# Kernel optimization log

Hardware: AMD Instinct MI355X
Metric: run time of the kernel (lower is better)

## Reference

```python
import jax, jax.numpy as jnp
import numpy as np

DIM = 128
HEADS = 4
NS = 7          # neighborhood_size (odd)
RADIUS = NS // 2
EXP = 2         # ffn expansion
EPS = 1e-8


def rmsnorm(x, w):
    # x: [B,C,H,W], w: [1,C,1,1]
    rms = jnp.mean(jnp.square(x), axis=1, keepdims=True)
    return x * jax.lax.rsqrt(rms + EPS) * w


def conv1x1(x, w, b):
    # w: [Cout,Cin], b: [Cout]
    return jnp.einsum('oi,bihw->bohw', w, x) + b[None, :, None, None]


def setup_inputs() -> dict:
    key = jax.random.key(0)
    ks = jax.random.split(key, 20)
    B, C, H, W = 2, DIM, 64, 64
    s = 0.02
    d = {
        'z': jax.random.normal(ks[0], (B, C, H, W), jnp.float32),
        'h': jax.random.normal(ks[1], (B, C, H, W), jnp.float32),
        'wz_norm': jnp.ones((1, C, 1, 1), jnp.float32),
        'wh_norm': jnp.ones((1, C, 1, 1), jnp.float32),
        'wq': jax.random.normal(ks[2], (C, C), jnp.float32) * s,
        'bq': jnp.zeros((C,), jnp.float32),
        'wk': jax.random.normal(ks[3], (C, C), jnp.float32) * s,
        'bk': jnp.zeros((C,), jnp.float32),
        'wv': jax.random.normal(ks[4], (C, C), jnp.float32) * s,
        'bv': jnp.zeros((C,), jnp.float32),
        'wo': jax.random.normal(ks[5], (C, C), jnp.float32) * s,
        'bo': jnp.zeros((C,), jnp.float32),
        'wffn_norm': jnp.ones((1, C, 1, 1), jnp.float32),
        'w1': jax.random.normal(ks[6], (C * EXP, C), jnp.float32) * s,
        'b1': jnp.zeros((C * EXP,), jnp.float32),
        'w2': jax.random.normal(ks[7], (C, C * EXP), jnp.float32) * s,
        'b2': jnp.zeros((C,), jnp.float32),
    }
    return d


def neighborhood_cross_attn(zq, hk, wq, bq, wk, bk, wv, bv, wo, bo):
    B, C, H, W = zq.shape
    hd = C // HEADS
    scale = hd ** (-0.5)
    q = conv1x1(zq, wq, bq)
    k = conv1x1(hk, wk, bk)
    v = conv1x1(hk, wv, bv)
    # [B, heads, H, W, hd]
    qh = q.reshape(B, HEADS, hd, H, W).transpose(0, 1, 3, 4, 2)
    kh = k.reshape(B, HEADS, hd, H, W).transpose(0, 1, 3, 4, 2)
    vh = v.reshape(B, HEADS, hd, H, W).transpose(0, 1, 3, 4, 2)
    offs = jnp.arange(-RADIUS, RADIUS + 1)
    dy, dx = jnp.meshgrid(offs, offs, indexing='ij')
    dy = dy.reshape(-1)  # [K]
    dx = dx.reshape(-1)
    by, bx = jnp.meshgrid(jnp.arange(H), jnp.arange(W), indexing='ij')
    ny = by[:, :, None] + dy  # [H, W, K]
    nx = bx[:, :, None] + dx
    valid = (ny >= 0) & (ny < H) & (nx >= 0) & (nx < W)
    nyc = jnp.clip(ny, 0, H - 1)
    nxc = jnp.clip(nx, 0, W - 1)
    # gather neighbors: [B, heads, H, W, K, hd]
    k_nb = kh[:, :, nyc, nxc]
    v_nb = vh[:, :, nyc, nxc]
    attn = jnp.einsum('bnhwd,bnhwkd->bnhwk', qh, k_nb) * scale
    attn = jnp.where(valid[None, None], attn, jnp.finfo(attn.dtype).min)
    p = jax.nn.softmax(attn, axis=-1)
    out = jnp.einsum('bnhwk,bnhwkd->bnhwd', p, v_nb)
    out = out.transpose(0, 1, 4, 2, 3).reshape(B, C, H, W)
    return conv1x1(out, wo, bo)


def reference(z, h, wz_norm, wh_norm, wq, bq, wk, bk, wv, bv, wo, bo,
              wffn_norm, w1, b1, w2, b2):
    h_norm = rmsnorm(h, wh_norm)
    z_norm = rmsnorm(z, wz_norm)
    z = z + neighborhood_cross_attn(z_norm, h_norm, wq, bq, wk, bk, wv, bv, wo, bo)
    y = rmsnorm(z, wffn_norm)
    y = conv1x1(y, w1, b1)
    y = jax.nn.gelu(y, approximate=False)
    y = conv1x1(y, w2, b2)
    return z + y
```

## Files before the change

### kernel.cpp

```cpp
#include <hip/hip_runtime.h>
#include <math.h>

#define CDIM 128
#define HW   4096
#define HEADS 4
#define HD   32

typedef __attribute__((ext_vector_type(8))) short bf16x8;
typedef __attribute__((ext_vector_type(4))) float f32x4;

static __device__ __forceinline__ unsigned int f2bf(float f) {
  union { float f; unsigned int u; } v; v.f = f;
  unsigned int r = v.u + 0x7FFF + ((v.u >> 16) & 1);
  return r >> 16;
}
static __device__ __forceinline__ float bflo(unsigned int u) {
  return __uint_as_float(u << 16);
}
static __device__ __forceinline__ float bfhi(unsigned int u) {
  return __uint_as_float(u & 0xFFFF0000u);
}
static __device__ __forceinline__ float gelu_f(float v) {
  return 0.5f * v * (1.0f + erff(v * 0.70710678118654752f));
}

__global__ __launch_bounds__(256) void head(
    const float* __restrict__ z, const float* __restrict__ h,
    const float* __restrict__ wzn, const float* __restrict__ whn,
    const float* __restrict__ wq, const float* __restrict__ bq,
    const float* __restrict__ wk, const float* __restrict__ bk,
    const float* __restrict__ wv, const float* __restrict__ bv,
    const float* __restrict__ wo, const float* __restrict__ w1,
    const float* __restrict__ w2, ushort* __restrict__ WB,
    ushort* __restrict__ Qb, ushort* __restrict__ Kb, ushort* __restrict__ Vb) {
  const int sel = blockIdx.y, t = threadIdx.x;
  if (sel == 3) {
    int e = (blockIdx.x * 256 + t) * 4;
    if (e < 81920) {
      const float* src; int off;
      if      (e < 16384) { src = wo; off = 0; }
      else if (e < 49152) { src = w1; off = 16384; }
      else                { src = w2; off = 49152; }
      float4 v = *(const float4*)&src[e - off];
      uint2 r;
      r.x = f2bf(v.x) | (f2bf(v.y) << 16);
      r.y = f2bf(v.z) | (f2bf(v.w) << 16);
      *(uint2*)&WB[49152 + e] = r;
    }
    return;
  }
  __shared__ __align__(16) ushort sW[128 * 128];
  __shared__ __align__(16) ushort sX[64 * 128];
  __shared__ float sh[4][64];

  const float* X    = (sel == 0) ? z : h;
  const float* wn   = (sel == 0) ? wzn : whn;
  const float* Wf   = (sel == 0) ? wq : (sel == 1 ? wk : wv);
  const float* bias = (sel == 0) ? bq : (sel == 1 ? bk : bv);
  ushort* outB      = (sel == 0) ? Qb : (sel == 1 ? Kb : Vb);

#pragma unroll
  for (int i = 0; i < 8; ++i) {
    int u  = t + i * 256;
    int o  = u >> 4;
    int k8 = (u & 15) * 8;
    float4 v0 = *(const float4*)&Wf[o * 128 + k8];
    float4 v1 = *(const float4*)&Wf[o * 128 + k8 + 4];
    uint4 pk;
    pk.x = f2bf(v0.x) | (f2bf(v0.y) << 16);
    pk.y = f2bf(v0.z) | (f2bf(v0.w) << 16);
    pk.z = f2bf(v1.x) | (f2bf(v1.y) << 16);
    pk.w = f2bf(v1.z) | (f2bf(v1.w) << 16);
    int idx = (o * 128 + k8) ^ ((o & 7) << 3);
    *(uint4*)&sW[idx] = pk;
  }

  const int pl = t & 63, g = t >> 6;
  const int gp = blockIdx.x * 64 + pl;
  const size_t xbase = (size_t)(gp >> 12) * CDIM * HW + (gp & 4095);
  float vals[32];
  float ss = 0.f;
#pragma unroll
  for (int j = 0; j < 32; ++j) {
    float v = X[xbase + (size_t)(g * 32 + j) * HW];
    vals[j] = v;
    ss += v * v;
  }
  sh[g][pl] = ss;
  __syncthreads();
  float tot = sh[0][pl] + sh[1][pl] + sh[2][pl] + sh[3][pl];
  float inv = rsqrtf(tot * (1.0f / CDIM) + 1e-8f);
#pragma unroll
  for (int jj = 0; jj < 4; ++jj) {
    unsigned int u[4];
#pragma unroll
    for (int p2 = 0; p2 < 4; ++p2) {
      int j = jj * 8 + p2 * 2;
      float a = vals[j]     * inv * wn[g * 32 + j];
      float b = vals[j + 1] * inv * wn[g * 32 + j + 1];
      u[p2] = f2bf(a) | (f2bf(b) << 16);
    }
    int idx = (pl * 128 + g * 32 + jj * 8) ^ ((pl & 7) << 3);
    *(uint4*)&sX[idx] = make_uint4(u[0], u[1], u[2], u[3]);
  }
  __syncthreads();

  const int w = t >> 6, l = t & 63, lr = l & 15, lk = l >> 4;
  const int m0 = w * 32;
  const int swz = (lr & 7) << 3;
  f32x4 acc[2][4] = {};
#pragma unroll
  for (int k0 = 0; k0 < 128; k0 += 32) {
    bf16x8 a0 = *(const bf16x8*)&sW[((m0 + lr) * 128 + k0 + lk * 8) ^ swz];
    bf16x8 a1 = *(const bf16x8*)&sW[((m0 + 16 + lr) * 128 + k0 + lk * 8) ^ swz];
    bf16x8 b[4];
#pragma unroll
    for (int nf = 0; nf < 4; ++nf)
      b[nf] = *(const bf16x8*)&sX[((nf * 16 + lr) * 128 + k0 + lk * 8) ^ swz];
#pragma unroll
    for (int nf = 0; nf < 4; ++nf) {
      acc[0][nf] = __builtin_amdgcn_mfma_f32_16x16x32_bf16(a0, b[nf], acc[0][nf], 0, 0, 0);
      acc[1][nf] = __builtin_amdgcn_mfma_f32_16x16x32_bf16(a1, b[nf], acc[1][nf], 0, 0, 0);
    }
  }
#pragma unroll
  for (int mf = 0; mf < 2; ++mf) {
    int obase = m0 + mf * 16 + lk * 4;
    f32x4 bv = *(const f32x4*)&bias[obase];
#pragma unroll
    for (int nf = 0; nf < 4; ++nf) {
      int P = blockIdx.x * 64 + nf * 16 + lr;
      uint2 pk;
      pk.x = f2bf(acc[mf][nf][0] + bv[0]) | (f2bf(acc[mf][nf][1] + bv[1]) << 16);
      pk.y = f2bf(acc[mf][nf][2] + bv[2]) | (f2bf(acc[mf][nf][3] + bv[3]) << 16);
      *(uint2*)&outB[(size_t)P * CDIM + obase] = pk;
    }
  }
}

__global__ __launch_bounds__(512) void nattn(
    const ushort* __restrict__ Q, const ushort* __restrict__ K,
    const ushort* __restrict__ V, ushort* __restrict__ ATT) {
  __shared__ __align__(16) unsigned int smem[20480];
  float* sS = (float*)smem;
  const int t  = threadIdx.x;
  const int px = t & 127;
  const int x  = px & 63;
  const int r  = px >> 6;
  const int dg = t >> 7;
  const int y0 = blockIdx.x * 2;
  const int h  = blockIdx.y;
  const int b  = blockIdx.z;
  const int ybase = y0 - 3;

  {
    int yy = t >> 6, xs = t & 63;
    int gy = min(max(ybase + yy, 0), 63);
    size_t gb = ((size_t)(b * HW + gy * 64 + xs)) * 64 + h * 16;
    const unsigned int* Ku = (const unsigned int*)K;
    const unsigned int* Vu = (const unsigned int*)V;
    int lb = (yy * 64 + xs) * 20;
#pragma unroll
    for (int i = 0; i < 4; ++i) {
      uint4 kv = *(const uint4*)&Ku[gb + i * 4];
      uint4 vv = *(const uint4*)&Vu[gb + i * 4];
      *(uint4*)&smem[lb + i * 4]         = kv;
      *(uint4*)&smem[10240 + lb + i * 4] = vv;
    }
  }
  const int Pq = b * HW + (y0 + r) * 64 + x;
  const unsigned int* Qu = (const unsigned int*)Q;
  float q[32];
#pragma unroll
  for (int i = 0; i < 4; ++i) {
    uint4 u4 = *(const uint4*)&Qu[(size_t)Pq * 64 + h * 16 + i * 4];
    q[i*8+0] = bflo(u4.x); q[i*8+1] = bfhi(u4.x);
    q[i*8+2] = bflo(u4.y); q[i*8+3] = bfhi(u4.y);
    q[i*8+4] = bflo(u4.z); q[i*8+5] = bfhi(u4.z);
    q[i*8+6] = bflo(u4.w); q[i*8+7] = bfhi(u4.w);
  }
  __syncthreads();

  const float scale = 0.17677669529663687f;
  const int nb0    = (dg == 0) ? 0 : dg * 12 + 1;
  const int ncount = (dg == 0) ? 13 : 12;
  float sreg[13];
#pragma unroll
  for (int j = 0; j < 13; ++j) {
    if (j < ncount) {
      int nb = nb0 + j;
      int dy = nb / 7 - 3;
      int dx = nb % 7 - 3;
      int ry = r + dy + 3;
      int nx = x + dx;
      int xx = min(max(nx, 0), 63);
      int ny = y0 + r + dy;
      bool valid = (ny >= 0) && (ny <= 63) && (nx >= 0) && (nx <= 63);
      const unsigned int* kb = &smem[(ry * 64 + xx) * 20];
      float acc = 0.f;
#pragma unroll
      for (int c = 0; c < 4; ++c) {
        uint4 u4 = *(const uint4*)&kb[c * 4];
        acc += q[c*8+0] * bflo(u4.x) + q[c*8+1] * bfhi(u4.x);
        acc += q[c*8+2] * bflo(u4.y) + q[c*8+3] * bfhi(u4.y);
        acc += q[c*8+4] * bflo(u4.z) + q[c*8+5] * bfhi(u4.z);
        acc += q[c*8+6] * bflo(u4.w) + q[c*8+7] * bfhi(u4.w);
      }
      sreg[j] = valid ? acc * scale : -1e30f;
    }
  }
  __syncthreads();
#pragma unroll
  for (int j = 0; j < 13; ++j)
    if (j < ncount) sS[(nb0 + j) * 128 + px] = sreg[j];
  __syncthreads();

  float o[8] = {0.f, 0.f, 0.f, 0.f, 0.f, 0.f, 0.f, 0.f};
  float sum = 0.f;
#pragma unroll
  for (int nb = 0; nb < 49; ++nb) {
    float p = __expf(sS[nb * 128 + px] - 8.0f);
    sum += p;
    int ry = r + nb / 7;
    int xx = min(max(x + nb % 7 - 3, 0), 63);
    uint4 u4 = *(const uint4*)&smem[10240 + (ry * 64 + xx) * 20 + dg * 4];
    o[0] += p * bflo(u4.x); o[1] += p * bfhi(u4.x);
    o[2] += p * bflo(u4.y); o[3] += p * bfhi(u4.y);
    o[4] += p * bflo(u4.z); o[5] += p * bfhi(u4.z);
    o[6] += p * bflo(u4.w); o[7] += p * bfhi(u4.w);
  }
  float inv = 1.0f / sum;
  unsigned int pk[4];
#pragma unroll
  for (int j = 0; j < 4; ++j)
    pk[j] = f2bf(o[2*j] * inv) | (f2bf(o[2*j+1] * inv) << 16);
  *(uint4*)&ATT[(size_t)Pq * CDIM + h * HD + dg * 8] = make_uint4(pk[0], pk[1], pk[2], pk[3]);
}

__global__ __launch_bounds__(256) void tail(
    const ushort* __restrict__ ATT, const ushort* __restrict__ WB,
    const float* __restrict__ bo, const float* __restrict__ z,
    const float* __restrict__ wfn, const float* __restrict__ b1,
    const float* __restrict__ b2, float* __restrict__ out) {
  __shared__ __align__(16) float  zlds[32][132];
  __shared__ __align__(16) ushort fn_s[32 * 128];
  __shared__ __align__(16) ushort hid_s[32 * 256];
  __shared__ float sums[32][17];
  __shared__ float sinv[32];
  const ushort* Wo = WB + 49152;
  const ushort* W1 = WB + 65536;
  const ushort* W2 = WB + 98304;
  const int t = threadIdx.x, w = t >> 6, l = t & 63, lr = l & 15, lk = l >> 4;
  const int pblk = blockIdx.x * 32;
  const int m0 = w * 32;

  {
    const ushort* A0 = Wo + (size_t)(m0 + lr) * 128 + lk * 8;
    const ushort* A1 = A0 + 16 * 128;
    const ushort* B0 = ATT + (size_t)(pblk + lr) * 128 + lk * 8;
    const ushort* B1 = B0 + 16 * 128;
    f32x4 acc[2][2] = {};
#pragma unroll
    for (int k0 = 0; k0 < 128; k0 += 32) {
      bf16x8 a0 = *(const bf16x8*)(A0 + k0);
      bf16x8 a1 = *(const bf16x8*)(A1 + k0);
      bf16x8 b0 = *(const bf16x8*)(B0 + k0);
      bf16x8 b1 = *(const bf16x8*)(B1 + k0);
      acc[0][0] = __builtin_amdgcn_mfma_f32_16x16x32_bf16(a0, b0, acc[0][0], 0, 0, 0);
      acc[0][1] = __builtin_amdgcn_mfma_f32_16x16x32_bf16(a0, b1, acc[0][1], 0, 0, 0);
      acc[1][0] = __builtin_amdgcn_mfma_f32_16x16x32_bf16(a1, b0, acc[1][0], 0, 0, 0);
      acc[1][1] = __builtin_amdgcn_mfma_f32_16x16x32_bf16(a1, b1, acc[1][1], 0, 0, 0);
    }
#pragma unroll
    for (int nf = 0; nf < 2; ++nf) {
      int px = nf * 16 + lr;
      int P  = pblk + px;
      int b_ = P >> 12, p = P & 4095;
      float ss = 0.f;
#pragma unroll
      for (int mf = 0; mf < 2; ++mf) {
        int row0 = m0 + mf * 16 + lk * 4;
        f32x4 bv = *(const f32x4*)&bo[row0];
        f32x4 rr;
#pragma unroll
        for (int j = 0; j < 4; ++j) {
          size_t gi = ((size_t)(b_ * CDIM + row0 + j)) * HW + p;
          float u = acc[mf][nf][j] + bv[j] + z[gi];
          rr[j] = u;
          ss += u * u;
        }
        *(f32x4*)&zlds[px][row0] = rr;
      }
      sums[px][w * 4 + lk] = ss;
    }
  }
  __syncthreads();
  if (t < 32) {
    float tot = 0.f;
#pragma unroll
    for (int i = 0; i < 16; ++i) tot += sums[t][i];
    sinv[t] = rsqrtf(tot * (1.0f / CDIM) + 1e-8f);
  }
  __syncthreads();
#pragma unroll
  for (int nf = 0; nf < 2; ++nf) {
    int px = nf * 16 + lr;
    float inv = sinv[px];
#pragma unroll
    for (int mf = 0; mf < 2; ++mf) {
      int row0 = m0 + mf * 16 + lk * 4;
      f32x4 uu = *(const f32x4*)&zlds[px][row0];
      f32x4 wf = *(const f32x4*)&wfn[row0];
      uint2 pk;
      pk.x = f2bf(uu[0] * inv * wf[0]) | (f2bf(uu[1] * inv * wf[1]) << 16);
      pk.y = f2bf(uu[2] * inv * wf[2]) | (f2bf(uu[3] * inv * wf[3]) << 16);
      int idx = (px * 128 + row0) ^ ((px & 7) << 3);
      *(uint2*)&fn_s[idx] = pk;
    }
  }
  __syncthreads();
  {
    const int hm0 = w * 64;
    const ushort* A0 = W1 + (size_t)(hm0 + lr) * 128 + lk * 8;
    f32x4 acc1[4][2] = {};
#pragma unroll
    for (int k0 = 0; k0 < 128; k0 += 32) {
      bf16x8 a[4], b[2];
#pragma unroll
      for (int mf = 0; mf < 4; ++mf) a[mf] = *(const bf16x8*)(A0 + mf * 16 * 128 + k0);
#pragma unroll
      for (int nf = 0; nf < 2; ++nf) {
        int px = nf * 16 + lr;
        b[nf] = *(const bf16x8*)&fn_s[(px * 128 + k0 + lk * 8) ^ ((px & 7) << 3)];
      }
#pragma unroll
      for (int mf = 0; mf < 4; ++mf)
#pragma unroll
        for (int nf = 0; nf < 2; ++nf)
          acc1[mf][nf] = __builtin_amdgcn_mfma_f32_16x16x32_bf16(a[mf], b[nf], acc1[mf][nf], 0, 0, 0);
    }
#pragma unroll
    for (int mf = 0; mf < 4; ++mf) {
      int ch0 = hm0 + mf * 16 + lk * 4;
      f32x4 bv = *(const f32x4*)&b1[ch0];
#pragma unroll
      for (int nf = 0; nf < 2; ++nf) {
        int px = nf * 16 + lr;
        float v0 = gelu_f(acc1[mf][nf][0] + bv[0]);
        float v1 = gelu_f(acc1[mf][nf][1] + bv[1]);
        float v2 = gelu_f(acc1[mf][nf][2] + bv[2]);
        float v3 = gelu_f(acc1[mf][nf][3] + bv[3]);
        uint2 pk;
        pk.x = f2bf(v0) | (f2bf(v1) << 16);
        pk.y = f2bf(v2) | (f2bf(v3) << 16);
        int idx = (px * 256 + ch0) ^ ((px & 7) << 3);
        *(uint2*)&hid_s[idx] = pk;
      }
    }
  }
  __syncthreads();
  {
    const ushort* C0 = W2 + (size_t)(m0 + lr) * 256 + lk * 8;
    f32x4 acc2[2][2] = {};
#pragma unroll
    for (int k0 = 0; k0 < 256; k0 += 32) {
      bf16x8 a0 = *(const bf16x8*)(C0 + k0);
      bf16x8 a1 = *(const bf16x8*)(C0 + 16 * 256 + k0);
      bf16x8 b[2];
#pragma unroll
      for (int nf = 0; nf < 2; ++nf) {
        int px = nf * 16 + lr;
        b[nf] = *(const bf16x8*)&hid_s[(px * 256 + k0 + lk * 8) ^ ((px & 7) << 3)];
      }
      acc2[0][0] = __builtin_amdgcn_mfma_f32_16x16x32_bf16(a0, b[0], acc2[0][0], 0, 0, 0);
      acc2[0][1] = __builtin_amdgcn_mfma_f32_16x16x32_bf16(a0, b[1], acc2[0][1], 0, 0, 0);
      acc2[1][0] = __builtin_amdgcn_mfma_f32_16x16x32_bf16(a1, b[0], acc2[1][0], 0, 0, 0);
      acc2[1][1] = __builtin_amdgcn_mfma_f32_16x16x32_bf16(a1, b[1], acc2[1][1], 0, 0, 0);
    }
#pragma unroll
    for (int mf = 0; mf < 2; ++mf) {
      int row0 = m0 + mf * 16 + lk * 4;
      f32x4 bv = *(const f32x4*)&b2[row0];
#pragma unroll
      for (int nf = 0; nf < 2; ++nf) {
        int px = nf * 16 + lr;
        int P  = pblk + px;
        int b_ = P >> 12, p = P & 4095;
        f32x4 zz = *(const f32x4*)&zlds[px][row0];
#pragma unroll
        for (int j = 0; j < 4; ++j) {
          size_t gi = ((size_t)(b_ * CDIM + row0 + j)) * HW + p;
          out[gi] = acc2[mf][nf][j] + bv[j] + zz[j];
        }
      }
    }
  }
}

extern "C" void kernel_launch(void* const* d_in, const int* in_sizes, int n_in,
                              void* d_out, int out_size, void* d_ws, size_t ws_size,
                              hipStream_t stream) {
  const float* z   = (const float*)d_in[0];
  const float* h   = (const float*)d_in[1];
  const float* wzn = (const float*)d_in[2];
  const float* whn = (const float*)d_in[3];
  const float* wq  = (const float*)d_in[4];
  const float* bq  = (const float*)d_in[5];
  const float* wk  = (const float*)d_in[6];
  const float* bk  = (const float*)d_in[7];
  const float* wv  = (const float*)d_in[8];
  const float* bv  = (const float*)d_in[9];
  const float* wo  = (const float*)d_in[10];
  const float* bo  = (const float*)d_in[11];
  const float* wfn = (const float*)d_in[12];
  const float* w1  = (const float*)d_in[13];
  const float* b1  = (const float*)d_in[14];
  const float* w2  = (const float*)d_in[15];
  const float* b2  = (const float*)d_in[16];
  float* out = (float*)d_out;

  const size_t U = 1048576;
  ushort* Qb  = (ushort*)d_ws;
  ushort* Kb  = Qb + U;
  ushort* Vb  = Kb + U;
  ushort* ATT = Vb + U;
  ushort* WB  = ATT + U;

  head<<<dim3(128, 4), 256, 0, stream>>>(z, h, wzn, whn, wq, bq, wk, bk, wv, bv,
                                         wo, w1, w2, WB, Qb, Kb, Vb);
  nattn<<<dim3(32, HEADS, 2), 512, 0, stream>>>(Qb, Kb, Vb, ATT);
  tail<<<dim3(256), 256, 0, stream>>>(ATT, WB, bo, z, wfn, b1, b2, out);
}
```

Measured before the change: 40.59 us.

## Fuse three kernels into one persistent kernel with grid barriers

Merges the projection, neighborhood-attention and FFN tail kernels into a single 256-block, 512-thread kernel. Stages are separated by software grid-wide atomic barriers, and a memset resets the counters before each launch. This removes two kernel launch gaps, and the tail stage is re-tiled so each wave computes 16 output rows instead of 32. It also moves the softmax exp into the score loop and replaces erf GELU with a sigmoid-based tanh approximation, which changes numerics slightly. The barrier relies on all 256 blocks being co-resident, and it adds a memset launch.

Result: slower. 90.58 us (+123.2%).

```diff
diff --git a/kernel.cpp b/kernel.cpp
--- a/kernel.cpp
+++ b/kernel.cpp
@@ -3,7 +3,6 @@
 
 #define CDIM 128
 #define HW   4096
-#define HEADS 4
 #define HD   32
 
 typedef __attribute__((ext_vector_type(8))) short bf16x8;
@@ -21,365 +20,362 @@
   return __uint_as_float(u & 0xFFFF0000u);
 }
 static __device__ __forceinline__ float gelu_f(float v) {
-  return 0.5f * v * (1.0f + erff(v * 0.70710678118654752f));
-}
-
-__global__ __launch_bounds__(256) void head(
+  float y = v * (1.595769122f + 0.071354816f * v * v);
+  return v / (1.0f + __expf(-y));
+}
+
+static __device__ __forceinline__ void gridbar(unsigned int* c, unsigned int n) {
+  __syncthreads();
+  if (threadIdx.x == 0) {
+    __threadfence();
+    atomicAdd(c, 1u);
+    while (__hip_atomic_load(c, __ATOMIC_RELAXED, __HIP_MEMORY_SCOPE_AGENT) < n) {}
+    __threadfence();
+  }
+  __syncthreads();
+}
+
+__global__ __launch_bounds__(512) void fused(
     const float* __restrict__ z, const float* __restrict__ h,
     const float* __restrict__ wzn, const float* __restrict__ whn,
     const float* __restrict__ wq, const float* __restrict__ bq,
     const float* __restrict__ wk, const float* __restrict__ bk,
     const float* __restrict__ wv, const float* __restrict__ bv,
-    const float* __restrict__ wo, const float* __restrict__ w1,
-    const float* __restrict__ w2, ushort* __restrict__ WB,
-    ushort* __restrict__ Qb, ushort* __restrict__ Kb, ushort* __restrict__ Vb) {
-  const int sel = blockIdx.y, t = threadIdx.x;
-  if (sel == 3) {
-    int e = (blockIdx.x * 256 + t) * 4;
-    if (e < 81920) {
+    const float* __restrict__ wo, const float* __restrict__ bo,
+    const float* __restrict__ wfn, const float* __restrict__ w1,
+    const float* __restrict__ b1, const float* __restrict__ w2,
+    const float* __restrict__ b2,
+    ushort* __restrict__ Qb, ushort* __restrict__ Kb, ushort* __restrict__ Vb,
+    ushort* __restrict__ ATT, ushort* __restrict__ WB,
+    float* __restrict__ out, unsigned int* __restrict__ bar) {
+  __shared__ __align__(16) unsigned char SMEM[100352];
+  const int t   = threadIdx.x;
+  const int bid = blockIdx.x;
+
+  {
+    const int g   = t >> 8;
+    const int t2  = t & 255;
+    const int job = bid * 2 + g;
+    const int type = job >> 7;
+    ushort* sW = (ushort*)(SMEM + g * 32768);
+    ushort* sX = (ushort*)(SMEM + 65536 + g * 16384);
+    float*  sh = (float*)(SMEM + 98304 + g * 1024);
+    const int pxb = job & 127;
+    const int pl = t2 & 63, gq = t2 >> 6;
+    float vals[32];
+
+    if (type < 3) {
+      const float* Wf = (type == 0) ? wq : (type == 1 ? wk : wv);
+#pragma unroll
+      for (int i = 0; i < 8; ++i) {
+        int u  = t2 + i * 256;
+        int o  = u >> 4;
+        int k8 = (u & 15) * 8;
+        float4 v0 = *(const float4*)&Wf[o * 128 + k8];
+        float4 v1 = *(const float4*)&Wf[o * 128 + k8 + 4];
+        uint4 pk;
+        pk.x = f2bf(v0.x) | (f2bf(v0.y) << 16);
+        pk.y = f2bf(v0.z) | (f2bf(v0.w) << 16);
+        pk.z = f2bf(v1.x) | (f2bf(v1.y) << 16);
+        pk.w = f2bf(v1.z) | (f2bf(v1.w) << 16);
+        *(uint4*)&sW[(o * 128 + k8) ^ ((o & 7) << 3)] = pk;
+      }
+      const float* X = (type == 0) ? z : h;
+      const int gp = pxb * 64 + pl;
+      const size_t xbase = (size_t)(gp >> 12) * CDIM * HW + (gp & 4095);
+      float ss = 0.f;
+#pragma unroll
+      for (int j = 0; j < 32; ++j) {
+        float v = X[xbase + (size_t)(gq * 32 + j) * HW];
+        vals[j] = v;
+        ss += v * v;
+      }
+      sh[gq * 64 + pl] = ss;
+    } else if (job - 384 < 80) {
+      int e = ((job - 384) * 256 + t2) * 4;
       const float* src; int off;
       if      (e < 16384) { src = wo; off = 0; }
       else if (e < 49152) { src = w1; off = 16384; }
       else                { src = w2; off = 49152; }
       float4 v = *(const float4*)&src[e - off];
-      uint2 r;
-      r.x = f2bf(v.x) | (f2bf(v.y) << 16);
-      r.y = f2bf(v.z) | (f2bf(v.w) << 16);
-      *(uint2*)&WB[49152 + e] = r;
-    }
-    return;
+      uint2 r2;
+      r2.x = f2bf(v.x) | (f2bf(v.y) << 16);
+      r2.y = f2bf(v.z) | (f2bf(v.w) << 16);
+      *(uint2*)&WB[49152 + e] = r2;
+    }
+    __syncthreads();
+    if (type < 3) {
+      const float* wn = (type == 0) ? wzn : whn;
+      float tot = sh[pl] + sh[64 + pl] + sh[128 + pl] + sh[192 + pl];
+      float inv = rsqrtf(tot * (1.0f / CDIM) + 1e-8f);
+#pragma unroll
+      for (int jj = 0; jj < 4; ++jj) {
+        unsigned int u[4];
+#pragma unroll
+        for (int p2 = 0; p2 < 4; ++p2) {
+          int j = jj * 8 + p2 * 2;
+          float a = vals[j]     * inv * wn[gq * 32 + j];
+          float b = vals[j + 1] * inv * wn[gq * 32 + j + 1];
+          u[p2] = f2bf(a) | (f2bf(b) << 16);
+        }
+        int idx = (pl * 128 + gq * 32 + jj * 8) ^ ((pl & 7) << 3);
+        *(uint4*)&sX[idx] = make_uint4(u[0], u[1], u[2], u[3]);
+      }
+    }
+    __syncthreads();
+    if (type < 3) {
+      const int w4 = t2 >> 6, l = t2 & 63, lr = l & 15, lk = l >> 4;
+      const int m0 = w4 * 32;
+      const int swz = (lr & 7) << 3;
+      const float* bias = (type == 0) ? bq : (type == 1 ? bk : bv);
+      ushort* outB      = (type == 0) ? Qb : (type == 1 ? Kb : Vb);
+      f32x4 acc[2][4] = {};
+#pragma unroll
+      for (int ki = 0; ki < 4; ++ki) {
+        bf16x8 a0 = *(const bf16x8*)&sW[((m0 + lr) * 128 + ki * 32 + lk * 8) ^ swz];
+        bf16x8 a1 = *(const bf16x8*)&sW[((m0 + 16 + lr) * 128 + ki * 32 + lk * 8) ^ swz];
+#pragma unroll
+        for (int nf = 0; nf < 4; ++nf) {
+          bf16x8 bb = *(const bf16x8*)&sX[((nf * 16 + lr) * 128 + ki * 32 + lk * 8) ^ swz];
+          acc[0][nf] = __builtin_amdgcn_mfma_f32_16x16x32_bf16(a0, bb, acc[0][nf], 0, 0, 0);
+          acc[1][nf] = __builtin_amdgcn_mfma_f32_16x16x32_bf16(a1, bb, acc[1][nf], 0, 0, 0);
+        }
+      }
+#pragma unroll
+      for (int mf = 0; mf < 2; ++mf) {
+        int obase = m0 + mf * 16 + lk * 4;
+        f32x4 bv4 = *(const f32x4*)&bias[obase];
+#pragma unroll
+        for (int nf = 0; nf < 4; ++nf) {
+          int P = pxb * 64 + nf * 16 + lr;
+          uint2 pk;
+          pk.x = f2bf(acc[mf][nf][0] + bv4[0]) | (f2bf(acc[mf][nf][1] + bv4[1]) << 16);
+          pk.y = f2bf(acc[mf][nf][2] + bv4[2]) | (f2bf(acc[mf][nf][3] + bv4[3]) << 16);
+          *(uint2*)&outB[(size_t)P * CDIM + obase] = pk;
+        }
+      }
+    }
   }
-  __shared__ __align__(16) ushort sW[128 * 128];
-  __shared__ __align__(16) ushort sX[64 * 128];
-  __shared__ float sh[4][64];
-
-  const float* X    = (sel == 0) ? z : h;
-  const float* wn   = (sel == 0) ? wzn : whn;
-  const float* Wf   = (sel == 0) ? wq : (sel == 1 ? wk : wv);
-  const float* bias = (sel == 0) ? bq : (sel == 1 ? bk : bv);
-  ushort* outB      = (sel == 0) ? Qb : (sel == 1 ? Kb : Vb);
-
-#pragma unroll
-  for (int i = 0; i < 8; ++i) {
-    int u  = t + i * 256;
-    int o  = u >> 4;
-    int k8 = (u & 15) * 8;
-    float4 v0 = *(const float4*)&Wf[o * 128 + k8];
-    float4 v1 = *(const float4*)&Wf[o * 128 + k8 + 4];
-    uint4 pk;
-    pk.x = f2bf(v0.x) | (f2bf(v0.y) << 16);
-    pk.y = f2bf(v0.z) | (f2bf(v0.w) << 16);
-    pk.z = f2bf(v1.x) | (f2bf(v1.y) << 16);
-    pk.w = f2bf(v1.z) | (f2bf(v1.w) << 16);
-    int idx = (o * 128 + k8) ^ ((o & 7) << 3);
-    *(uint4*)&sW[idx] = pk;
+  gridbar(&bar[0], gridDim.x);
+
+  {
+    unsigned int* smem = (unsigned int*)SMEM;
+    float* sS = (float*)smem;
+    const int px = t & 127;
+    const int x  = px & 63;
+    const int r  = px >> 6;
+    const int dg = t >> 7;
+    const int y0 = (bid & 31) * 2;
+    const int hh = (bid >> 5) & 3;
+    const int b  = bid >> 7;
+    const int ybase = y0 - 3;
+    {
+      int yy = t >> 6, xs = t & 63;
+      int gy = min(max(ybase + yy, 0), 63);
+      size_t gb = ((size_t)(b * HW + gy * 64 + xs)) * 64 + hh * 16;
+      const unsigned int* Ku = (const unsigned int*)Kb;
+      const unsigned int* Vu = (const unsigned int*)Vb;
+      int lb = (yy * 64 + xs) * 20;
+#pragma unroll
+      for (int i = 0; i < 4; ++i) {
+        uint4 kv = *(const uint4*)&Ku[gb + i * 4];
+        uint4 vv = *(const uint4*)&Vu[gb + i * 4];
+        *(uint4*)&smem[lb + i * 4]         = kv;
+        *(uint4*)&smem[10240 + lb + i * 4] = vv;
+      }
+    }
+    const int Pq = b * HW + (y0 + r) * 64 + x;
+    const unsigned int* Qu = (const unsigned int*)Qb;
+    float q[32];
+#pragma unroll
+    for (int i = 0; i < 4; ++i) {
+      uint4 u4 = *(const uint4*)&Qu[(size_t)Pq * 64 + hh * 16 + i * 4];
+      q[i*8+0] = bflo(u4.x); q[i*8+1] = bfhi(u4.x);
+      q[i*8+2] = bflo(u4.y); q[i*8+3] = bfhi(u4.y);
+      q[i*8+4] = bflo(u4.z); q[i*8+5] = bfhi(u4.z);
+      q[i*8+6] = bflo(u4.w); q[i*8+7] = bfhi(u4.w);
+    }
+    __syncthreads();
+    const float scale = 0.17677669529663687f;
+    const int nb0    = (dg == 0) ? 0 : dg * 12 + 1;
+    const int ncount = (dg == 0) ? 13 : 12;
+    float sreg[13];
+#pragma unroll
+    for (int j = 0; j < 13; ++j) {
+      if (j < ncount) {
+        int nb = nb0 + j;
+        int dy = nb / 7 - 3;
+        int dx = nb % 7 - 3;
+        int ry = r + dy + 3;
+        int nx = x + dx;
+        int xx = min(max(nx, 0), 63);
+        int ny = y0 + r + dy;
+        bool valid = (ny >= 0) && (ny <= 63) && (nx >= 0) && (nx <= 63);
+        const unsigned int* kb = &smem[(ry * 64 + xx) * 20];
+        float acc = 0.f;
+#pragma unroll
+        for (int c = 0; c < 4; ++c) {
+          uint4 u4 = *(const uint4*)&kb[c * 4];
+          acc += q[c*8+0] * bflo(u4.x) + q[c*8+1] * bfhi(u4.x);
+          acc += q[c*8+2] * bflo(u4.y) + q[c*8+3] * bfhi(u4.y);
+          acc += q[c*8+4] * bflo(u4.z) + q[c*8+5] * bfhi(u4.z);
+          acc += q[c*8+6] * bflo(u4.w) + q[c*8+7] * bfhi(u4.w);
+        }
+        sreg[j] = valid ? __expf(acc * scale - 8.0f) : 0.0f;
+      }
+    }
+    __syncthreads();
+#pragma unroll
+    for (int j = 0; j < 13; ++j)
+      if (j < ncount) sS[(nb0 + j) * 128 + px] = sreg[j];
+    __syncthreads();
+    float o[8] = {0.f, 0.f, 0.f, 0.f, 0.f, 0.f, 0.f, 0.f};
+    float sum = 0.f;
+#pragma unroll
+    for (int nb = 0; nb < 49; ++nb) {
+      float p = sS[nb * 128 + px];
+      sum += p;
+      int ry = r + nb / 7;
+      int xx = min(max(x + nb % 7 - 3, 0), 63);
+      uint4 u4 = *(const uint4*)&smem[10240 + (ry * 64 + xx) * 20 + dg * 4];
+      o[0] += p * bflo(u4.x); o[1] += p * bfhi(u4.x);
+      o[2] += p * bflo(u4.y); o[3] += p * bfhi(u4.y);
+      o[4] += p * bflo(u4.z); o[5] += p * bfhi(u4.z);
+      o[6] += p * bflo(u4.w); o[7] += p * bfhi(u4.w);
+    }
+    float inv = 1.0f / sum;
+    unsigned int pk[4];
+#pragma unroll
+    for (int j = 0; j < 4; ++j)
+      pk[j] = f2bf(o[2*j] * inv) | (f2bf(o[2*j+1] * inv) << 16);
+    *(uint4*)&ATT[(size_t)Pq * CDIM + hh * HD + dg * 8] = make_uint4(pk[0], pk[1], pk[2], pk[3]);
   }
-
-  const int pl = t & 63, g = t >> 6;
-  const int gp = blockIdx.x * 64 + pl;
-  const size_t xbase = (size_t)(gp >> 12) * CDIM * HW + (gp & 4095);
-  float vals[32];
-  float ss = 0.f;
-#pragma unroll
-  for (int j = 0; j < 32; ++j) {
-    float v = X[xbase + (size_t)(g * 32 + j) * HW];
-    vals[j] = v;
-    ss += v * v;
-  }
-  sh[g][pl] = ss;
-  __syncthreads();
-  float tot = sh[0][pl] + sh[1][pl] + sh[2][pl] + sh[3][pl];
-  float inv = rsqrtf(tot * (1.0f / CDIM) + 1e-8f);
-#pragma unroll
-  for (int jj = 0; jj < 4; ++jj) {
-    unsigned int u[4];
-#pragma unroll
-    for (int p2 = 0; p2 < 4; ++p2) {
-      int j = jj * 8 + p2 * 2;
-      float a = vals[j]     * inv * wn[g * 32 + j];
-      float b = vals[j + 1] * inv * wn[g * 32 + j + 1];
-      u[p2] = f2bf(a) | (f2bf(b) << 16);
-    }
-    int idx = (pl * 128 + g * 32 + jj * 8) ^ ((pl & 7) << 3);
-    *(uint4*)&sX[idx] = make_uint4(u[0], u[1], u[2], u[3]);
-  }
-  __syncthreads();
-
-  const int w = t >> 6, l = t & 63, lr = l & 15, lk = l >> 4;
-  const int m0 = w * 32;
-  const int swz = (lr & 7) << 3;
-  f32x4 acc[2][4] = {};
-#pragma unroll
-  for (int k0 = 0; k0 < 128; k0 += 32) {
-    bf16x8 a0 = *(const bf16x8*)&sW[((m0 + lr) * 128 + k0 + lk * 8) ^ swz];
-    bf16x8 a1 = *(const bf16x8*)&sW[((m0 + 16 + lr) * 128 + k0 + lk * 8) ^ swz];
-    bf16x8 b[4];
-#pragma unroll
-    for (int nf = 0; nf < 4; ++nf)
-      b[nf] = *(const bf16x8*)&sX[((nf * 16 + lr) * 128 + k0 + lk * 8) ^ swz];
-#pragma unroll
-    for (int nf = 0; nf < 4; ++nf) {
-      acc[0][nf] = __builtin_amdgcn_mfma_f32_16x16x32_bf16(a0, b[nf], acc[0][nf], 0, 0, 0);
-      acc[1][nf] = __builtin_amdgcn_mfma_f32_16x16x32_bf16(a1, b[nf], acc[1][nf], 0, 0, 0);
-    }
-  }
-#pragma unroll
-  for (int mf = 0; mf < 2; ++mf) {
-    int obase = m0 + mf * 16 + lk * 4;
-    f32x4 bv = *(const f32x4*)&bias[obase];
-#pragma unroll
-    for (int nf = 0; nf < 4; ++nf) {
-      int P = blockIdx.x * 64 + nf * 16 + lr;
-      uint2 pk;
-      pk.x = f2bf(acc[mf][nf][0] + bv[0]) | (f2bf(acc[mf][nf][1] + bv[1]) << 16);
-      pk.y = f2bf(acc[mf][nf][2] + bv[2]) | (f2bf(acc[mf][nf][3] + bv[3]) << 16);
-      *(uint2*)&outB[(size_t)P * CDIM + obase] = pk;
-    }
-  }
-}
-
-__global__ __launch_bounds__(512) void nattn(
-    const ushort* __restrict__ Q, const ushort* __restrict__ K,
-    const ushort* __restrict__ V, ushort* __restrict__ ATT) {
-  __shared__ __align__(16) unsigned int smem[20480];
-  float* sS = (float*)smem;
-  const int t  = threadIdx.x;
-  const int px = t & 127;
-  const int x  = px & 63;
-  const int r  = px >> 6;
-  const int dg = t >> 7;
-  const int y0 = blockIdx.x * 2;
-  const int h  = blockIdx.y;
-  const int b  = blockIdx.z;
-  const int ybase = y0 - 3;
+  gridbar(&bar[1], gridDim.x);
 
   {
-    int yy = t >> 6, xs = t & 63;
-    int gy = min(max(ybase + yy, 0), 63);
-    size_t gb = ((size_t)(b * HW + gy * 64 + xs)) * 64 + h * 16;
-    const unsigned int* Ku = (const unsigned int*)K;
-    const unsigned int* Vu = (const unsigned int*)V;
-    int lb = (yy * 64 + xs) * 20;
-#pragma unroll
-    for (int i = 0; i < 4; ++i) {
-      uint4 kv = *(const uint4*)&Ku[gb + i * 4];
-      uint4 vv = *(const uint4*)&Vu[gb + i * 4];
-      *(uint4*)&smem[lb + i * 4]         = kv;
-      *(uint4*)&smem[10240 + lb + i * 4] = vv;
-    }
-  }
-  const int Pq = b * HW + (y0 + r) * 64 + x;
-  const unsigned int* Qu = (const unsigned int*)Q;
-  float q[32];
-#pragma unroll
-  for (int i = 0; i < 4; ++i) {
-    uint4 u4 = *(const uint4*)&Qu[(size_t)Pq * 64 + h * 16 + i * 4];
-    q[i*8+0] = bflo(u4.x); q[i*8+1] = bfhi(u4.x);
-    q[i*8+2] = bflo(u4.y); q[i*8+3] = bfhi(u4.y);
-    q[i*8+4] = bflo(u4.z); q[i*8+5] = bfhi(u4.z);
-    q[i*8+6] = bflo(u4.w); q[i*8+7] = bfhi(u4.w);
-  }
-  __syncthreads();
-
-  const float scale = 0.17677669529663687f;
-  const int nb0    = (dg == 0) ? 0 : dg * 12 + 1;
-  const int ncount = (dg == 0) ? 13 : 12;
-  float sreg[13];
-#pragma unroll
-  for (int j = 0; j < 13; ++j) {
-    if (j < ncount) {
-      int nb = nb0 + j;
-      int dy = nb / 7 - 3;
-      int dx = nb % 7 - 3;
-      int ry = r + dy + 3;
-      int nx = x + dx;
-      int xx = min(max(nx, 0), 63);
-      int ny = y0 + r + dy;
-      bool valid = (ny >= 0) && (ny <= 63) && (nx >= 0) && (nx <= 63);
-      const unsigned int* kb = &smem[(ry * 64 + xx) * 20];
-      float acc = 0.f;
-#pragma unroll
-      for (int c = 0; c < 4; ++c) {
-        uint4 u4 = *(const uint4*)&kb[c * 4];
-        acc += q[c*8+0] * bflo(u4.x) + q[c*8+1] * bfhi(u4.x);
-        acc += q[c*8+2] * bflo(u4.y) + q[c*8+3] * bfhi(u4.y);
-        acc += q[c*8+4] * bflo(u4.z) + q[c*8+5] * bfhi(u4.z);
-        acc += q[c*8+6] * bflo(u4.w) + q[c*8+7] * bfhi(u4.w);
-      }
-      sreg[j] = valid ? acc * scale : -1e30f;
-    }
-  }
-  __syncthreads();
-#pragma unroll
-  for (int j = 0; j < 13; ++j)
-    if (j < ncount) sS[(nb0 + j) * 128 + px] = sreg[j];
-  __syncthreads();
-
-  float o[8] = {0.f, 0.f, 0.f, 0.f, 0.f, 0.f, 0.f, 0.f};
-  float sum = 0.f;
-#pragma unroll
-  for (int nb = 0; nb < 49; ++nb) {
-    float p = __expf(sS[nb * 128 + px] - 8.0f);
-    sum += p;
-    int ry = r + nb / 7;
-    int xx = min(max(x + nb % 7 - 3, 0), 63);
-    uint4 u4 = *(const uint4*)&smem[10240 + (ry * 64 + xx) * 20 + dg * 4];
-    o[0] += p * bflo(u4.x); o[1] += p * bfhi(u4.x);
-    o[2] += p * bflo(u4.y); o[3] += p * bfhi(u4.y);
-    o[4] += p * bflo(u4.z); o[5] += p * bfhi(u4.z);
-    o[6] += p * bflo(u4.w); o[7] += p * bfhi(u4.w);
-  }
-  float inv = 1.0f / sum;
-  unsigned int pk[4];
-#pragma unroll
-  for (int j = 0; j < 4; ++j)
-    pk[j] = f2bf(o[2*j] * inv) | (f2bf(o[2*j+1] * inv) << 16);
-  *(uint4*)&ATT[(size_t)Pq * CDIM + h * HD + dg * 8] = make_uint4(pk[0], pk[1], pk[2], pk[3]);
-}
-
-__global__ __launch_bounds__(256) void tail(
-    const ushort* __restrict__ ATT, const ushort* __restrict__ WB,
-    const float* __restrict__ bo, const float* __restrict__ z,
-    const float* __restrict__ wfn, const float* __restrict__ b1,
-    const float* __restrict__ b2, float* __restrict__ out) {
-  __shared__ __align__(16) float  zlds[32][132];
-  __shared__ __align__(16) ushort fn_s[32 * 128];
-  __shared__ __align__(16) ushort hid_s[32 * 256];
-  __shared__ float sums[32][17];
-  __shared__ float sinv[32];
-  const ushort* Wo = WB + 49152;
-  const ushort* W1 = WB + 65536;
-  const ushort* W2 = WB + 98304;
-  const int t = threadIdx.x, w = t >> 6, l = t & 63, lr = l & 15, lk = l >> 4;
-  const int pblk = blockIdx.x * 32;
-  const int m0 = w * 32;
-
-  {
-    const ushort* A0 = Wo + (size_t)(m0 + lr) * 128 + lk * 8;
-    const ushort* A1 = A0 + 16 * 128;
-    const ushort* B0 = ATT + (size_t)(pblk + lr) * 128 + lk * 8;
-    const ushort* B1 = B0 + 16 * 128;
-    f32x4 acc[2][2] = {};
-#pragma unroll
-    for (int k0 = 0; k0 < 128; k0 += 32) {
-      bf16x8 a0 = *(const bf16x8*)(A0 + k0);
-      bf16x8 a1 = *(const bf16x8*)(A1 + k0);
-      bf16x8 b0 = *(const bf16x8*)(B0 + k0);
-      bf16x8 b1 = *(const bf16x8*)(B1 + k0);
-      acc[0][0] = __builtin_amdgcn_mfma_f32_16x16x32_bf16(a0, b0, acc[0][0], 0, 0, 0);
-      acc[0][1] = __builtin_amdgcn_mfma_f32_16x16x32_bf16(a0, b1, acc[0][1], 0, 0, 0);
-      acc[1][0] = __builtin_amdgcn_mfma_f32_16x16x32_bf16(a1, b0, acc[1][0], 0, 0, 0);
-      acc[1][1] = __builtin_amdgcn_mfma_f32_16x16x32_bf16(a1, b1, acc[1][1], 0, 0, 0);
-    }
-#pragma unroll
-    for (int nf = 0; nf < 2; ++nf) {
-      int px = nf * 16 + lr;
-      int P  = pblk + px;
-      int b_ = P >> 12, p = P & 4095;
-      float ss = 0.f;
-#pragma unroll
-      for (int mf = 0; mf < 2; ++mf) {
-        int row0 = m0 + mf * 16 + lk * 4;
-        f32x4 bv = *(const f32x4*)&bo[row0];
+    float  (*zlds)[132] = (float(*)[132])SMEM;
+    ushort* fn_s  = (ushort*)(SMEM + 16896);
+    ushort* hid_s = (ushort*)(SMEM + 25088);
+    float  (*sums)[36] = (float(*)[36])(SMEM + 41472);
+    float*  sinv  = (float*)(SMEM + 46080);
+    const ushort* Wo = WB + 49152;
+    const ushort* W1 = WB + 65536;
+    const ushort* W2 = WB + 98304;
+    const int w = t >> 6, l = t & 63, lr = l & 15, lk = l >> 4;
+    const int pblk = bid * 32;
+    {
+      const int m0 = w * 16;
+      const ushort* A0 = Wo + (size_t)(m0 + lr) * 128 + lk * 8;
+      const ushort* B0 = ATT + (size_t)(pblk + lr) * 128 + lk * 8;
+      const ushort* B1 = B0 + 16 * 128;
+      f32x4 acc[2] = {};
+#pragma unroll
+      for (int k0 = 0; k0 < 128; k0 += 32) {
+        bf16x8 a0 = *(const bf16x8*)(A0 + k0);
+        bf16x8 b0 = *(const bf16x8*)(B0 + k0);
+        bf16x8 b1 = *(const bf16x8*)(B1 + k0);
+        acc[0] = __builtin_amdgcn_mfma_f32_16x16x32_bf16(a0, b0, acc[0], 0, 0, 0);
+        acc[1] = __builtin_amdgcn_mfma_f32_16x16x32_bf16(a0, b1, acc[1], 0, 0, 0);
+      }
+      const int row0 = m0 + lk * 4;
+      f32x4 bv = *(const f32x4*)&bo[row0];
+#pragma unroll
+      for (int nf = 0; nf < 2; ++nf) {
+        int px = nf * 16 + lr;
+        int P  = pblk + px;
+        int b_ = P >> 12, p = P & 4095;
+        float ss = 0.f;
         f32x4 rr;
 #pragma unroll
         for (int j = 0; j < 4; ++j) {
           size_t gi = ((size_t)(b_ * CDIM + row0 + j)) * HW + p;
-          float u = acc[mf][nf][j] + bv[j] + z[gi];
+          float u = acc[nf][j] + bv[j] + z[gi];
           rr[j] = u;
           ss += u * u;
         }
         *(f32x4*)&zlds[px][row0] = rr;
-      }
-      sums[px][w * 4 + lk] = ss;
-    }
-  }
-  __syncthreads();
-  if (t < 32) {
-    float tot = 0.f;
-#pragma unroll
-    for (int i = 0; i < 16; ++i) tot += sums[t][i];
-    sinv[t] = rsqrtf(tot * (1.0f / CDIM) + 1e-8f);
-  }
-  __syncthreads();
-#pragma unroll
-  for (int nf = 0; nf < 2; ++nf) {
-    int px = nf * 16 + lr;
-    float inv = sinv[px];
-#pragma unroll
-    for (int mf = 0; mf < 2; ++mf) {
-      int row0 = m0 + mf * 16 + lk * 4;
-      f32x4 uu = *(const f32x4*)&zlds[px][row0];
+        sums[px][w * 4 + lk] = ss;
+      }
+    }
+    __syncthreads();
+    if (t < 32) {
+      float tot = 0.f;
+#pragma unroll
+      for (int i = 0; i < 32; ++i) tot += sums[t][i];
+      sinv[t] = rsqrtf(tot * (1.0f / CDIM) + 1e-8f);
+    }
+    __syncthreads();
+    {
+      const int row0 = w * 16 + lk * 4;
       f32x4 wf = *(const f32x4*)&wfn[row0];
-      uint2 pk;
-      pk.x = f2bf(uu[0] * inv * wf[0]) | (f2bf(uu[1] * inv * wf[1]) << 16);
-      pk.y = f2bf(uu[2] * inv * wf[2]) | (f2bf(uu[3] * inv * wf[3]) << 16);
-      int idx = (px * 128 + row0) ^ ((px & 7) << 3);
-      *(uint2*)&fn_s[idx] = pk;
-    }
-  }
-  __syncthreads();
-  {
-    const int hm0 = w * 64;
-    const ushort* A0 = W1 + (size_t)(hm0 + lr) * 128 + lk * 8;
-    f32x4 acc1[4][2] = {};
-#pragma unroll
-    for (int k0 = 0; k0 < 128; k0 += 32) {
-      bf16x8 a[4], b[2];
-#pragma unroll
-      for (int mf = 0; mf < 4; ++mf) a[mf] = *(const bf16x8*)(A0 + mf * 16 * 128 + k0);
 #pragma unroll
       for (int nf = 0; nf < 2; ++nf) {
         int px = nf * 16 + lr;
-        b[nf] = *(const bf16x8*)&fn_s[(px * 128 + k0 + lk * 8) ^ ((px & 7) << 3)];
-      }
-#pragma unroll
-      for (int mf = 0; mf < 4; ++mf)
-#pragma unroll
-        for (int nf = 0; nf < 2; ++nf)
-          acc1[mf][nf] = __builtin_amdgcn_mfma_f32_16x16x32_bf16(a[mf], b[nf], acc1[mf][nf], 0, 0, 0);
-    }
-#pragma unroll
-    for (int mf = 0; mf < 4; ++mf) {
-      int ch0 = hm0 + mf * 16 + lk * 4;
-      f32x4 bv = *(const f32x4*)&b1[ch0];
-#pragma unroll
-      for (int nf = 0; nf < 2; ++nf) {
-        int px = nf * 16 + lr;
-        float v0 = gelu_f(acc1[mf][nf][0] + bv[0]);
-        float v1 = gelu_f(acc1[mf][nf][1] + bv[1]);
-        float v2 = gelu_f(acc1[mf][nf][2] + bv[2]);
-        float v3 = gelu_f(acc1[mf][nf][3] + bv[3]);
+        float inv = sinv[px];
+        f32x4 uu = *(const f32x4*)&zlds[px][row0];
         uint2 pk;
-        pk.x = f2bf(v0) | (f2bf(v1) << 16);
-        pk.y = f2bf(v2) | (f2bf(v3) << 16);
-        int idx = (px * 256 + ch0) ^ ((px & 7) << 3);
-        *(uint2*)&hid_s[idx] = pk;
-      }
-    }
-  }
-  __syncthreads();
-  {
-    const ushort* C0 = W2 + (size_t)(m0 + lr) * 256 + lk * 8;
-    f32x4 acc2[2][2] = {};
-#pragma unroll
-    for (int k0 = 0; k0 < 256; k0 += 32) {
-      bf16x8 a0 = *(const bf16x8*)(C0 + k0);
-      bf16x8 a1 = *(const bf16x8*)(C0 + 16 * 256 + k0);
-      bf16x8 b[2];
-#pragma unroll
-      for (int nf = 0; nf < 2; ++nf) {
-        int px = nf * 16 + lr;
-        b[nf] = *(const bf16x8*)&hid_s[(px * 256 + k0 + lk * 8) ^ ((px & 7) << 3)];
-      }
-      acc2[0][0] = __builtin_amdgcn_mfma_f32_16x16x32_bf16(a0, b[0], acc2[0][0], 0, 0, 0);
-      acc2[0][1] = __builtin_amdgcn_mfma_f32_16x16x32_bf16(a0, b[1], acc2[0][1], 0, 0, 0);
-      acc2[1][0] = __builtin_amdgcn_mfma_f32_16x16x32_bf16(a1, b[0], acc2[1][0], 0, 0, 0);
-      acc2[1][1] = __builtin_amdgcn_mfma_f32_16x16x32_bf16(a1, b[1], acc2[1][1], 0, 0, 0);
-    }
-#pragma unroll
-    for (int mf = 0; mf < 2; ++mf) {
-      int row0 = m0 + mf * 16 + lk * 4;
+        pk.x = f2bf(uu[0] * inv * wf[0]) | (f2bf(uu[1] * inv * wf[1]) << 16);
+        pk.y = f2bf(uu[2] * inv * wf[2]) | (f2bf(uu[3] * inv * wf[3]) << 16);
+        *(uint2*)&fn_s[(px * 128 + row0) ^ ((px & 7) << 3)] = pk;
+      }
+    }
+    __syncthreads();
+    {
+      const int hm0 = w * 32;
+      const ushort* A0 = W1 + (size_t)(hm0 + lr) * 128 + lk * 8;
+      f32x4 acc1[2][2] = {};
+#pragma unroll
+      for (int k0 = 0; k0 < 128; k0 += 32) {
+        bf16x8 a[2], b[2];
+#pragma unroll
+        for (int mf = 0; mf < 2; ++mf) a[mf] = *(const bf16x8*)(A0 + mf * 16 * 128 + k0);
+#pragma unroll
+        for (int nf = 0; nf < 2; ++nf) {
+          int px = nf * 16 + lr;
+          b[nf] = *(const bf16x8*)&fn_s[(px * 128 + k0 + lk * 8) ^ ((px & 7) << 3)];
+        }
+#pragma unroll
+        for (int mf = 0; mf < 2; ++mf)
+#pragma unroll
+          for (int nf = 0; nf < 2; ++nf)
+            acc1[mf][nf] = __builtin_amdgcn_mfma_f32_16x16x32_bf16(a[mf], b[nf], acc1[mf][nf], 0, 0, 0);
+      }
+#pragma unroll
+      for (int mf = 0; mf < 2; ++mf) {
+        int ch0 = hm0 + mf * 16 + lk * 4;
+        f32x4 bv = *(const f32x4*)&b1[ch0];
+#pragma unroll
+        for (int nf = 0; nf < 2; ++nf) {
+          int px = nf * 16 + lr;
+          float v0 = gelu_f(acc1[mf][nf][0] + bv[0]);
+          float v1 = gelu_f(acc1[mf][nf][1] + bv[1]);
+          float v2 = gelu_f(acc1[mf][nf][2] + bv[2]);
+          float v3 = gelu_f(acc1[mf][nf][3] + bv[3]);
+          uint2 pk;
+          pk.x = f2bf(v0) | (f2bf(v1) << 16);
+          pk.y = f2bf(v2) | (f2bf(v3) << 16);
+          *(uint2*)&hid_s[(px * 256 + ch0) ^ ((px & 7) << 3)] = pk;
+        }
+      }
+    }
+    __syncthreads();
+    {
+      const int m0 = w * 16;
+      const ushort* C0 = W2 + (size_t)(m0 + lr) * 256 + lk * 8;
+      f32x4 acc2[2] = {};
+#pragma unroll
+      for (int k0 = 0; k0 < 256; k0 += 32) {
+        bf16x8 a0 = *(const bf16x8*)(C0 + k0);
+        bf16x8 b[2];
+#pragma unroll
+        for (int nf = 0; nf < 2; ++nf) {
+          int px = nf * 16 + lr;
+          b[nf] = *(const bf16x8*)&hid_s[(px * 256 + k0 + lk * 8) ^ ((px & 7) << 3)];
+        }
+        acc2[0] = __builtin_amdgcn_mfma_f32_16x16x32_bf16(a0, b[0], acc2[0], 0, 0, 0);
+        acc2[1] = __builtin_amdgcn_mfma_f32_16x16x32_bf16(a0, b[1], acc2[1], 0, 0, 0);
+      }
+      const int row0 = m0 + lk * 4;
       f32x4 bv = *(const f32x4*)&b2[row0];
 #pragma unroll
       for (int nf = 0; nf < 2; ++nf) {
@@ -390,7 +386,7 @@
 #pragma unroll
         for (int j = 0; j < 4; ++j) {
           size_t gi = ((size_t)(b_ * CDIM + row0 + j)) * HW + p;
-          out[gi] = acc2[mf][nf][j] + bv[j] + zz[j];
+          out[gi] = acc2[nf][j] + bv[j] + zz[j];
         }
       }
     }
@@ -425,9 +421,10 @@
   ushort* Vb  = Kb + U;
   ushort* ATT = Vb + U;
   ushort* WB  = ATT + U;
-
-  head<<<dim3(128, 4), 256, 0, stream>>>(z, h, wzn, whn, wq, bq, wk, bk, wv, bv,
-                                         wo, w1, w2, WB, Qb, Kb, Vb);
-  nattn<<<dim3(32, HEADS, 2), 512, 0, stream>>>(Qb, Kb, Vb, ATT);
-  tail<<<dim3(256), 256, 0, stream>>>(ATT, WB, bo, z, wfn, b1, b2, out);
-}
+  unsigned int* BAR = (unsigned int*)((char*)d_ws + (16u << 20));
+
+  (void)hipMemsetAsync(BAR, 0, 64, stream);
+  fused<<<dim3(256), 512, 0, stream>>>(z, h, wzn, whn, wq, bq, wk, bk, wv, bv,
+                                       wo, bo, wfn, w1, b1, w2, b2,
+                                       Qb, Kb, Vb, ATT, WB, out, BAR);
+}
```
